# Kernel tuning notes

Measured on AMD Instinct MI355X. Metric: run time of the kernel, lower is better.

Reference implementation:

```python
import jax, jax.numpy as jnp
import numpy as np

B, S, DIM = 2, 2048, 512
NH, QK, VD = 8, 128, 128
NEG = -1e9


def setup_inputs() -> dict:
    key = jax.random.key(0)
    ks = jax.random.split(key, 10)
    scale = 0.02
    x = jax.random.normal(ks[0], (B, S, DIM), dtype=jnp.float32)
    pos_embedding = jax.random.normal(ks[1], (NH, S, S), dtype=jnp.float32) * scale
    # causal additive mask: 0 on/below diagonal, large negative above
    mask = jnp.where(jnp.tril(jnp.ones((S, S), dtype=bool)), 0.0, NEG).astype(jnp.float32)
    wq_w = jax.random.normal(ks[2], (DIM, NH * QK), dtype=jnp.float32) * scale
    wq_b = jax.random.normal(ks[3], (NH * QK,), dtype=jnp.float32) * scale
    wk_w = jax.random.normal(ks[4], (DIM, NH * QK), dtype=jnp.float32) * scale
    wk_b = jax.random.normal(ks[5], (NH * QK,), dtype=jnp.float32) * scale
    wv_w = jax.random.normal(ks[6], (DIM, NH * VD), dtype=jnp.float32) * scale
    wv_b = jax.random.normal(ks[7], (NH * VD,), dtype=jnp.float32) * scale
    wo_w = jax.random.normal(ks[8], (NH * VD, DIM), dtype=jnp.float32) * scale
    wo_b = jax.random.normal(ks[9], (DIM,), dtype=jnp.float32) * scale
    return {
        "x": x, "start_pos": 0, "mask": mask, "pos_embedding": pos_embedding,
        "wq_w": wq_w, "wq_b": wq_b, "wk_w": wk_w, "wk_b": wk_b,
        "wv_w": wv_w, "wv_b": wv_b, "wo_w": wo_w, "wo_b": wo_b,
    }


def reference(x, start_pos, mask, pos_embedding,
              wq_w, wq_b, wk_w, wk_b, wv_w, wv_b, wo_w, wo_b):
    b, s, _ = x.shape
    # per-head positional bias slice [NH, s, s]
    pe = pos_embedding[:, start_pos:start_pos + s, start_pos:start_pos + s]
    q = (x @ wq_w + wq_b).reshape(b, s, NH, QK)
    k = (x @ wk_w + wk_b).reshape(b, s, NH, QK)
    v = (x @ wv_w + wv_b).reshape(b, s, NH, VD)
    # unfused attention: full [b, h, s, S] score tensor
    score = jnp.einsum('bshk,bShk->bhsS', q, k) / np.float32(np.sqrt(QK))
    score = score + pe[None] + mask[None, None, :s, :s]
    score = jax.nn.softmax(score, axis=-1).astype(x.dtype)
    out = jnp.einsum('bhsS,bShv->bshv', score, v).reshape(b, s, NH * VD)
    return out @ wo_w + wo_b
```

## Files before the change

### kernel.cpp

```cpp
#include <hip/hip_runtime.h>
#include <hip/hip_bf16.h>
#include <stdint.h>

#define BB_ 2
#define SS_ 2048
#define DIM_ 512
#define NH_ 8
#define QK_ 128
#define VD_ 128

typedef __attribute__((ext_vector_type(8))) short bf16x8;
typedef __attribute__((ext_vector_type(4))) float f32x4;
typedef __attribute__((ext_vector_type(8))) unsigned short ushort8;
typedef __attribute__((ext_vector_type(4))) unsigned short ushort4v;

__device__ __forceinline__ unsigned short f2bf(float f) {
  union { float f; unsigned int u; } v; v.f = f;
  unsigned int r = v.u + 0x7FFFu + ((v.u >> 16) & 1u);
  return (unsigned short)(r >> 16);
}

__device__ __forceinline__ float bf2f(unsigned short u) {
  union { unsigned int u; float f; } v; v.u = ((unsigned int)u) << 16;
  return v.f;
}

__device__ __forceinline__ f32x4 mfma16(bf16x8 a, bf16x8 b, f32x4 c) {
  return __builtin_amdgcn_mfma_f32_16x16x32_bf16(a, b, c, 0, 0, 0);
}


__device__ void transpose_tile(const float* __restrict__ src, unsigned short* __restrict__ dst,
                               int R, int C, int c0, int r0, int tid, float (*t)[65]) {
  const int rr = tid >> 4, cc4 = (tid & 15) * 4;
#pragma unroll
  for (int p = 0; p < 4; p++) {
    float4 v = *reinterpret_cast<const float4*>(src + (size_t)(r0 + rr + p * 16) * C + c0 + cc4);
    t[rr + p * 16][cc4 + 0] = v.x; t[rr + p * 16][cc4 + 1] = v.y;
    t[rr + p * 16][cc4 + 2] = v.z; t[rr + p * 16][cc4 + 3] = v.w;
  }
  __syncthreads();
  const int cl = tid >> 2, rb = (tid & 3) * 16;
#pragma unroll
  for (int g = 0; g < 2; g++) {
    ushort8 o;
#pragma unroll
    for (int j = 0; j < 8; j++) o[j] = f2bf(t[rb + g * 8 + j][cl]);
    *reinterpret_cast<ushort8*>(dst + (size_t)(c0 + cl) * R + r0 + rb + g * 8) = o;
  }
}

__global__ void k_prep(const float* __restrict__ x, unsigned short* __restrict__ xb,
                       const float* __restrict__ wq, const float* __restrict__ wk,
                       const float* __restrict__ wv, unsigned short* __restrict__ wqkv_t,
                       const float* __restrict__ wo, unsigned short* __restrict__ wo_t,
                       const float* __restrict__ bq, const float* __restrict__ bk,
                       const float* __restrict__ bv, float* __restrict__ bias_out) {
  __shared__ float t[64][65];
  const int bid = blockIdx.x, tid = threadIdx.x;
  if (bid < 2048) {
    const int i = bid * 256 + tid;
    float4 v = reinterpret_cast<const float4*>(x)[i];
    ushort4v o;
    o[0] = f2bf(v.x); o[1] = f2bf(v.y); o[2] = f2bf(v.z); o[3] = f2bf(v.w);
    reinterpret_cast<ushort4v*>(xb)[i] = o;
  } else if (bid < 2432) {
    const int tt0 = bid - 2048;
    const int w = tt0 >> 7, tt = tt0 & 127;
    const float* src = (w == 0) ? wq : (w == 1) ? wk : wv;
    transpose_tile(src, wqkv_t + (size_t)w * 1024 * 512, 512, 1024,
                   (tt & 15) * 64, (tt >> 4) * 64, tid, t);
  } else if (bid < 2560) {
    const int tt = bid - 2432;
    transpose_tile(wo, wo_t, 1024, 512, (tt & 7) * 64, (tt >> 3) * 64, tid, t);
  } else {
    const int i = (bid - 2560) * 256 + tid;
    if (i < 1024) bias_out[i] = bq[i];
    else if (i < 2048) bias_out[i] = bk[i - 1024];
    else if (i < 3072) bias_out[i] = bv[i - 2048];
  }
}


template <int EPI>
__global__ __launch_bounds__(256) void k_gemm_bt(
    const unsigned short* __restrict__ A, const unsigned short* __restrict__ BT,
    const float* __restrict__ bias, int K,
    unsigned short* __restrict__ oq, unsigned short* __restrict__ ok,
    unsigned short* __restrict__ ovt, float* __restrict__ of) {
  __shared__ __align__(16) unsigned short Al[128][32];
  __shared__ __align__(16) unsigned short Bl[128][32];
  const int tid = threadIdx.x;
  const int lane = tid & 63, wave = tid >> 6;
  const int wm = wave >> 1, wn = wave & 1;
  const int lr = lane & 15, lg = lane >> 4;
  const int m0 = blockIdx.y * 128, n0 = blockIdx.x * 128;
  f32x4 acc[4][4] = {};
  const int srow = lane >> 2, scol = (lane & 3) * 8;

  for (int k0 = 0; k0 < K; k0 += 32) {
    __syncthreads();
    {
      const unsigned short* ga = A + (size_t)(m0 + wave * 16 + srow) * K + k0 + scol;
      __builtin_amdgcn_global_load_lds((const unsigned int*)ga,
                                       (unsigned int*)&Al[wave * 16][0], 16, 0, 0);
      __builtin_amdgcn_global_load_lds((const unsigned int*)(ga + (size_t)64 * K),
                                       (unsigned int*)&Al[wave * 16 + 64][0], 16, 0, 0);
      const unsigned short* gb = BT + (size_t)(n0 + wave * 16 + srow) * K + k0 + scol;
      __builtin_amdgcn_global_load_lds((const unsigned int*)gb,
                                       (unsigned int*)&Bl[wave * 16][0], 16, 0, 0);
      __builtin_amdgcn_global_load_lds((const unsigned int*)(gb + (size_t)64 * K),
                                       (unsigned int*)&Bl[wave * 16 + 64][0], 16, 0, 0);
    }
    __syncthreads();
    bf16x8 af[4], bfr[4];
#pragma unroll
    for (int i = 0; i < 4; i++)
      af[i] = *reinterpret_cast<const bf16x8*>(&Al[wm * 64 + i * 16 + lr][lg * 8]);
#pragma unroll
    for (int i = 0; i < 4; i++)
      bfr[i] = *reinterpret_cast<const bf16x8*>(&Bl[wn * 64 + i * 16 + lr][lg * 8]);
#pragma unroll
    for (int i = 0; i < 4; i++)
#pragma unroll
      for (int j = 0; j < 4; j++)
        acc[i][j] = mfma16(af[i], bfr[j], acc[i][j]);
  }

#pragma unroll
  for (int i = 0; i < 4; i++) {
#pragma unroll
    for (int j = 0; j < 4; j++) {
      const int n = n0 + wn * 64 + j * 16 + lr;
      const float bv = bias[n];
      const int mb = m0 + wm * 64 + i * 16 + lg * 4;
      if (EPI == 0) {
        const int region = n >> 10;
        const int h = (n & 1023) >> 7, d = n & 127;
        const int bb = mb >> 11, s0 = mb & 2047;
        const size_t hb = (size_t)(bb * NH_ + h) << 18;
        if (region == 2) {
          ushort4v pk;
#pragma unroll
          for (int r = 0; r < 4; r++) pk[r] = f2bf(acc[i][j][r] + bv);
          const int s32 = s0 >> 5, sg = (s0 >> 3) & 3, e0 = s0 & 7;
          const size_t off = hb + (size_t)(((s32 * 8 + (d >> 4)) * 4 + sg) * 128 + (d & 15) * 8 + e0);
          *reinterpret_cast<ushort4v*>(ovt + off) = pk;
        } else {
          unsigned short* dst = ((region == 0) ? oq : ok) + hb;
          const float qs = (region == 0) ? 0.08838834764831845f : 1.0f;
          const int rt_ = s0 >> 4, c_ = d >> 5, lg_ = (d >> 3) & 3, e_ = d & 7;
          const int lrb = s0 & 15;
#pragma unroll
          for (int r = 0; r < 4; r++)
            dst[(size_t)(((rt_ * 4 + c_) * 64 + lg_ * 16 + lrb + r) * 8 + e_)] =
                f2bf((acc[i][j][r] + bv) * qs);
        }
      } else {
#pragma unroll
        for (int r = 0; r < 4; r++) {
          const int m = mb + r;
          of[(size_t)m * DIM_ + n] = acc[i][j][r] + bv;
        }
      }
    }
  }
}


__global__ __launch_bounds__(256, 2) void k_attn(
    const unsigned short* __restrict__ q, const unsigned short* __restrict__ k,
    const unsigned short* __restrict__ vt, const float* __restrict__ pe,
    unsigned short* __restrict__ att) {
  __shared__ __align__(16) unsigned short P[4][2][16][72];
  __shared__ __align__(16) unsigned short Xo[4][32][136];
  __shared__ float Xml[4][32];

  const int h = blockIdx.x, p = blockIdx.y, b = blockIdx.z;
  const int lane = threadIdx.x & 63, wave = threadIdx.x >> 6;
  const int lr = lane & 15, lg = lane >> 4;

  const size_t hb = (size_t)(b * NH_ + h) << 18;
  const unsigned short* qfp = q + hb;
  const unsigned short* kfp = k + hb;
  const unsigned short* vfp = vt + hb;
  const float* peh = pe + (size_t)h * SS_ * SS_;

  for (int phase = 0; phase < 2; phase++) {
    const int rt = phase ? (63 - p) : p;
    const int myq0 = rt * 32 + lr;
    const float* pep = peh + (size_t)myq0 * SS_;

    bf16x8 qf[2][4];
#pragma unroll
    for (int t = 0; t < 2; t++)
#pragma unroll
      for (int c = 0; c < 4; c++)
        qf[t][c] = *reinterpret_cast<const bf16x8*>(
            qfp + ((size_t)((rt * 2 + t) * 4 + c) << 9) + (lane << 3));

    f32x4 o[2][8] = {};
    float l[2] = {0.f, 0.f};

    const int nkt = (rt >> 1) + 1;
    const int kt_lo = (nkt * wave) >> 2;
    const int kt_hi = (nkt * (wave + 1)) >> 2;

    for (int kt = kt_lo; kt < kt_hi; kt++) {
      const int kbase = kt * 64;

      f32x4 sc[2][4];
#pragma unroll
      for (int t = 0; t < 2; t++)
#pragma unroll
        for (int ck = 0; ck < 4; ck++)
          sc[t][ck] = *reinterpret_cast<const f32x4*>(
              pep + (size_t)(t * 16) * SS_ + kbase + ck * 16 + lg * 4);

      __builtin_amdgcn_s_setprio(1);
#pragma unroll
      for (int ck = 0; ck < 4; ck++) {
#pragma unroll
        for (int c = 0; c < 4; c++) {
          const bf16x8 kf = *reinterpret_cast<const bf16x8*>(
              kfp + ((size_t)((kt * 4 + ck) * 4 + c) << 9) + (lane << 3));
          sc[0][ck] = mfma16(kf, qf[0][c], sc[0][ck]);
          sc[1][ck] = mfma16(kf, qf[1][c], sc[1][ck]);
        }
      }
      __builtin_amdgcn_s_setprio(0);

      bf16x8 vf[8];
#pragma unroll
      for (int sub = 0; sub < 8; sub++)
        vf[sub] = *reinterpret_cast<const bf16x8*>(
            vfp + ((size_t)((kt * 2) * 8 + sub) << 9) + (lane << 3));

      const bool diag = (kt == nkt - 1);
#pragma unroll
      for (int t = 0; t < 2; t++) {
        const int mq = myq0 + t * 16;
        float rs0 = 0.f, rs1 = 0.f;
#pragma unroll
        for (int ck = 0; ck < 4; ck++) {
#pragma unroll
          for (int r = 0; r < 4; r++) {
            float v = sc[t][ck][r];
            if (diag && (kbase + ck * 16 + lg * 4 + r) > mq) v = -1e30f;
            const float pv = __expf(v);
            sc[t][ck][r] = pv;
            if (ck & 1) rs1 += pv; else rs0 += pv;
          }
        }
        l[t] += rs0 + rs1;
#pragma unroll
        for (int ck = 0; ck < 4; ck++) {
          ushort4v pk;
#pragma unroll
          for (int r = 0; r < 4; r++) pk[r] = f2bf(sc[t][ck][r]);
          *reinterpret_cast<ushort4v*>(&P[wave][t][lr][ck * 16 + lg * 4]) = pk;
        }
      }

      __builtin_amdgcn_s_setprio(1);
#pragma unroll
      for (int t = 0; t < 2; t++) {
        const bf16x8 pf = *reinterpret_cast<const bf16x8*>(&P[wave][t][lr][lg * 8]);
#pragma unroll
        for (int sub = 0; sub < 8; sub++)
          o[t][sub] = mfma16(vf[sub], pf, o[t][sub]);
      }
      __builtin_amdgcn_s_setprio(0);
#pragma unroll
      for (int sub = 0; sub < 8; sub++)
        vf[sub] = *reinterpret_cast<const bf16x8*>(
            vfp + ((size_t)((kt * 2 + 1) * 8 + sub) << 9) + (lane << 3));
      __builtin_amdgcn_s_setprio(1);
#pragma unroll
      for (int t = 0; t < 2; t++) {
        const bf16x8 pf = *reinterpret_cast<const bf16x8*>(&P[wave][t][lr][32 + lg * 8]);
#pragma unroll
        for (int sub = 0; sub < 8; sub++)
          o[t][sub] = mfma16(vf[sub], pf, o[t][sub]);
      }
      __builtin_amdgcn_s_setprio(0);
    }

#pragma unroll
    for (int t = 0; t < 2; t++) {
      l[t] += __shfl_xor(l[t], 16);
      l[t] += __shfl_xor(l[t], 32);
    }

#pragma unroll
    for (int t = 0; t < 2; t++) {
      const float inv = (l[t] > 0.f) ? 1.0f / l[t] : 0.f;
#pragma unroll
      for (int sub = 0; sub < 8; sub++) {
        ushort4v pk;
#pragma unroll
        for (int r = 0; r < 4; r++) pk[r] = f2bf(o[t][sub][r] * inv);
        *reinterpret_cast<ushort4v*>(&Xo[wave][t * 16 + lr][sub * 16 + lg * 4]) = pk;
      }
      if (lg == 0) Xml[wave][t * 16 + lr] = l[t];
    }
    __syncthreads();

    {
      const int mrow = wave * 8 + (lane >> 3);
      float c[4], csum = 0.f;
#pragma unroll
      for (int w = 0; w < 4; w++) { c[w] = Xml[w][mrow]; csum += c[w]; }
      const float invT = 1.0f / csum;
#pragma unroll
      for (int half = 0; half < 2; half++) {
        const int dc = (lane & 7) + half * 8;
        float acc[8] = {};
#pragma unroll
        for (int w = 0; w < 4; w++) {
          const ushort8 v = *reinterpret_cast<const ushort8*>(&Xo[w][mrow][dc * 8]);
#pragma unroll
          for (int e = 0; e < 8; e++) acc[e] += c[w] * bf2f(v[e]);
        }
        ushort8 outv;
#pragma unroll
        for (int e = 0; e < 8; e++) outv[e] = f2bf(acc[e] * invT);
        *reinterpret_cast<ushort8*>(
            att + (size_t)(b * SS_ + rt * 32 + mrow) * (NH_ * VD_) + h * VD_ + dc * 8) = outv;
      }
    }
    __syncthreads();
  }
}


extern "C" void kernel_launch(void* const* d_in, const int* in_sizes, int n_in,
                              void* d_out, int out_size, void* d_ws, size_t ws_size,
                              hipStream_t stream) {
  const float* x    = (const float*)d_in[0];
  const float* pe   = (const float*)d_in[3];
  const float* wq_w = (const float*)d_in[4];
  const float* wq_b = (const float*)d_in[5];
  const float* wk_w = (const float*)d_in[6];
  const float* wk_b = (const float*)d_in[7];
  const float* wv_w = (const float*)d_in[8];
  const float* wv_b = (const float*)d_in[9];
  const float* wo_w = (const float*)d_in[10];
  const float* wo_b = (const float*)d_in[11];
  float* out = (float*)d_out;

  char* ws = (char*)d_ws;
  unsigned short* x_bf   = (unsigned short*)(ws);
  unsigned short* wqkv_t = (unsigned short*)(ws + 4194304);
  unsigned short* wo_t   = (unsigned short*)(ws + 7340032);
  float*          qkv_b  = (float*)(ws + 8388608);
  unsigned short* qb     = (unsigned short*)(ws + 8400896);
  unsigned short* kb     = (unsigned short*)(ws + 16789504);
  unsigned short* vtb    = (unsigned short*)(ws + 25178112);
  unsigned short* attb   = (unsigned short*)(ws + 33566720);

  k_prep<<<2572, 256, 0, stream>>>(x, x_bf, wq_w, wk_w, wv_w, wqkv_t,
                                   wo_w, wo_t, wq_b, wk_b, wv_b, qkv_b);

  dim3 g1(24, 32);
  k_gemm_bt<0><<<g1, 256, 0, stream>>>(x_bf, wqkv_t, qkv_b, 512, qb, kb, vtb, nullptr);

  dim3 g2(NH_, 32, BB_);
  k_attn<<<g2, 256, 0, stream>>>(qb, kb, vtb, pe, attb);

  dim3 g3(4, 32);
  k_gemm_bt<1><<<g3, 256, 0, stream>>>(attb, wo_t, wo_b, 1024, nullptr, nullptr, nullptr, out);
}
```

Measured before the change: 103.1 us.

## Split attention key range across six waves with aliased shared buffers

The attention block grows from 4 to 6 waves, each handling a sixth of the causal key tiles, so more waves are available to hide memory latency. The P staging buffer and the per-wave output buffer now share one aliased shared-memory array, which requires an extra barrier before the output stage. The score computation is also split into two half-tiles, and V loads are issued in groups of four to lower register pressure. The costs are a larger six-way final reduction, two idle waves during the combine, and possible load imbalance when a query tile has few key tiles to divide among six waves.

New measurement: 122.3 us. +18.7%, slower.

```diff
diff --git a/kernel.cpp b/kernel.cpp
--- a/kernel.cpp
+++ b/kernel.cpp
@@ -168,13 +168,15 @@
 }
 
 
-__global__ __launch_bounds__(256, 2) void k_attn(
+#define PIDX(w, t, r, c)  ((((w) * 2 + (t)) * 16 + (r)) * 72 + (c))
+#define XIDX(w, r, c)     (((w) * 32 + (r)) * 136 + (c))
+
+__global__ __launch_bounds__(384, 2) void k_attn(
     const unsigned short* __restrict__ q, const unsigned short* __restrict__ k,
     const unsigned short* __restrict__ vt, const float* __restrict__ pe,
     unsigned short* __restrict__ att) {
-  __shared__ __align__(16) unsigned short P[4][2][16][72];
-  __shared__ __align__(16) unsigned short Xo[4][32][136];
-  __shared__ float Xml[4][32];
+  __shared__ __align__(16) unsigned short SH[26112];
+  __shared__ float Xml[6][32];
 
   const int h = blockIdx.x, p = blockIdx.y, b = blockIdx.z;
   const int lane = threadIdx.x & 63, wave = threadIdx.x >> 6;
@@ -203,87 +205,83 @@
     float l[2] = {0.f, 0.f};
 
     const int nkt = (rt >> 1) + 1;
-    const int kt_lo = (nkt * wave) >> 2;
-    const int kt_hi = (nkt * (wave + 1)) >> 2;
+    const int kt_lo = (nkt * wave) / 6;
+    const int kt_hi = (nkt * (wave + 1)) / 6;
 
     for (int kt = kt_lo; kt < kt_hi; kt++) {
       const int kbase = kt * 64;
-
-      f32x4 sc[2][4];
-#pragma unroll
-      for (int t = 0; t < 2; t++)
-#pragma unroll
-        for (int ck = 0; ck < 4; ck++)
-          sc[t][ck] = *reinterpret_cast<const f32x4*>(
-              pep + (size_t)(t * 16) * SS_ + kbase + ck * 16 + lg * 4);
-
-      __builtin_amdgcn_s_setprio(1);
-#pragma unroll
-      for (int ck = 0; ck < 4; ck++) {
-#pragma unroll
-        for (int c = 0; c < 4; c++) {
-          const bf16x8 kf = *reinterpret_cast<const bf16x8*>(
-              kfp + ((size_t)((kt * 4 + ck) * 4 + c) << 9) + (lane << 3));
-          sc[0][ck] = mfma16(kf, qf[0][c], sc[0][ck]);
-          sc[1][ck] = mfma16(kf, qf[1][c], sc[1][ck]);
-        }
-      }
-      __builtin_amdgcn_s_setprio(0);
-
-      bf16x8 vf[8];
-#pragma unroll
-      for (int sub = 0; sub < 8; sub++)
-        vf[sub] = *reinterpret_cast<const bf16x8*>(
-            vfp + ((size_t)((kt * 2) * 8 + sub) << 9) + (lane << 3));
-
       const bool diag = (kt == nkt - 1);
-#pragma unroll
-      for (int t = 0; t < 2; t++) {
-        const int mq = myq0 + t * 16;
-        float rs0 = 0.f, rs1 = 0.f;
-#pragma unroll
-        for (int ck = 0; ck < 4; ck++) {
-#pragma unroll
-          for (int r = 0; r < 4; r++) {
-            float v = sc[t][ck][r];
-            if (diag && (kbase + ck * 16 + lg * 4 + r) > mq) v = -1e30f;
-            const float pv = __expf(v);
-            sc[t][ck][r] = pv;
-            if (ck & 1) rs1 += pv; else rs0 += pv;
+
+#pragma unroll
+      for (int ckh = 0; ckh < 2; ckh++) {
+        f32x4 sch[2][2];
+#pragma unroll
+        for (int t = 0; t < 2; t++)
+#pragma unroll
+          for (int cc = 0; cc < 2; cc++)
+            sch[t][cc] = *reinterpret_cast<const f32x4*>(
+                pep + (size_t)(t * 16) * SS_ + kbase + (ckh * 2 + cc) * 16 + lg * 4);
+
+        __builtin_amdgcn_s_setprio(1);
+#pragma unroll
+        for (int cc = 0; cc < 2; cc++) {
+          const int ck = ckh * 2 + cc;
+#pragma unroll
+          for (int c = 0; c < 4; c++) {
+            const bf16x8 kf = *reinterpret_cast<const bf16x8*>(
+                kfp + ((size_t)((kt * 4 + ck) * 4 + c) << 9) + (lane << 3));
+            sch[0][cc] = mfma16(kf, qf[0][c], sch[0][cc]);
+            sch[1][cc] = mfma16(kf, qf[1][c], sch[1][cc]);
           }
         }
-        l[t] += rs0 + rs1;
-#pragma unroll
-        for (int ck = 0; ck < 4; ck++) {
-          ushort4v pk;
-#pragma unroll
-          for (int r = 0; r < 4; r++) pk[r] = f2bf(sc[t][ck][r]);
-          *reinterpret_cast<ushort4v*>(&P[wave][t][lr][ck * 16 + lg * 4]) = pk;
-        }
-      }
-
-      __builtin_amdgcn_s_setprio(1);
-#pragma unroll
-      for (int t = 0; t < 2; t++) {
-        const bf16x8 pf = *reinterpret_cast<const bf16x8*>(&P[wave][t][lr][lg * 8]);
-#pragma unroll
-        for (int sub = 0; sub < 8; sub++)
-          o[t][sub] = mfma16(vf[sub], pf, o[t][sub]);
-      }
-      __builtin_amdgcn_s_setprio(0);
-#pragma unroll
-      for (int sub = 0; sub < 8; sub++)
-        vf[sub] = *reinterpret_cast<const bf16x8*>(
-            vfp + ((size_t)((kt * 2 + 1) * 8 + sub) << 9) + (lane << 3));
-      __builtin_amdgcn_s_setprio(1);
-#pragma unroll
-      for (int t = 0; t < 2; t++) {
-        const bf16x8 pf = *reinterpret_cast<const bf16x8*>(&P[wave][t][lr][32 + lg * 8]);
-#pragma unroll
-        for (int sub = 0; sub < 8; sub++)
-          o[t][sub] = mfma16(vf[sub], pf, o[t][sub]);
-      }
-      __builtin_amdgcn_s_setprio(0);
+        __builtin_amdgcn_s_setprio(0);
+
+#pragma unroll
+        for (int t = 0; t < 2; t++) {
+          const int mq = myq0 + t * 16;
+          float rs = 0.f;
+#pragma unroll
+          for (int cc = 0; cc < 2; cc++) {
+            const int ck = ckh * 2 + cc;
+#pragma unroll
+            for (int r = 0; r < 4; r++) {
+              float v = sch[t][cc][r];
+              if (diag && (kbase + ck * 16 + lg * 4 + r) > mq) v = -1e30f;
+              const float pv = __expf(v);
+              sch[t][cc][r] = pv;
+              rs += pv;
+            }
+            ushort4v pk;
+#pragma unroll
+            for (int r = 0; r < 4; r++) pk[r] = f2bf(sch[t][cc][r]);
+            *reinterpret_cast<ushort4v*>(&SH[PIDX(wave, t, lr, ck * 16 + lg * 4)]) = pk;
+          }
+          l[t] += rs;
+        }
+      }
+
+#pragma unroll
+      for (int kk = 0; kk < 2; kk++) {
+        bf16x8 pf[2];
+#pragma unroll
+        for (int t = 0; t < 2; t++)
+          pf[t] = *reinterpret_cast<const bf16x8*>(&SH[PIDX(wave, t, lr, kk * 32 + lg * 8)]);
+#pragma unroll
+        for (int sg = 0; sg < 2; sg++) {
+          bf16x8 vf4[4];
+#pragma unroll
+          for (int s4 = 0; s4 < 4; s4++)
+            vf4[s4] = *reinterpret_cast<const bf16x8*>(
+                vfp + ((size_t)((kt * 2 + kk) * 8 + sg * 4 + s4) << 9) + (lane << 3));
+          __builtin_amdgcn_s_setprio(1);
+#pragma unroll
+          for (int t = 0; t < 2; t++)
+#pragma unroll
+            for (int s4 = 0; s4 < 4; s4++)
+              o[t][sg * 4 + s4] = mfma16(vf4[s4], pf[t], o[t][sg * 4 + s4]);
+          __builtin_amdgcn_s_setprio(0);
+        }
+      }
     }
 
 #pragma unroll
@@ -292,6 +290,8 @@
       l[t] += __shfl_xor(l[t], 32);
     }
 
+    __syncthreads();
+
 #pragma unroll
     for (int t = 0; t < 2; t++) {
       const float inv = (l[t] > 0.f) ? 1.0f / l[t] : 0.f;
@@ -300,25 +300,25 @@
         ushort4v pk;
 #pragma unroll
         for (int r = 0; r < 4; r++) pk[r] = f2bf(o[t][sub][r] * inv);
-        *reinterpret_cast<ushort4v*>(&Xo[wave][t * 16 + lr][sub * 16 + lg * 4]) = pk;
+        *reinterpret_cast<ushort4v*>(&SH[XIDX(wave, t * 16 + lr, sub * 16 + lg * 4)]) = pk;
       }
       if (lg == 0) Xml[wave][t * 16 + lr] = l[t];
     }
     __syncthreads();
 
-    {
+    if (wave < 4) {
       const int mrow = wave * 8 + (lane >> 3);
-      float c[4], csum = 0.f;
-#pragma unroll
-      for (int w = 0; w < 4; w++) { c[w] = Xml[w][mrow]; csum += c[w]; }
+      float c[6], csum = 0.f;
+#pragma unroll
+      for (int w = 0; w < 6; w++) { c[w] = Xml[w][mrow]; csum += c[w]; }
       const float invT = 1.0f / csum;
 #pragma unroll
       for (int half = 0; half < 2; half++) {
         const int dc = (lane & 7) + half * 8;
         float acc[8] = {};
 #pragma unroll
-        for (int w = 0; w < 4; w++) {
-          const ushort8 v = *reinterpret_cast<const ushort8*>(&Xo[w][mrow][dc * 8]);
+        for (int w = 0; w < 6; w++) {
+          const ushort8 v = *reinterpret_cast<const ushort8*>(&SH[XIDX(w, mrow, dc * 8)]);
 #pragma unroll
           for (int e = 0; e < 8; e++) acc[e] += c[w] * bf2f(v[e]);
         }
@@ -366,7 +366,7 @@
   k_gemm_bt<0><<<g1, 256, 0, stream>>>(x_bf, wqkv_t, qkv_b, 512, qb, kb, vtb, nullptr);
 
   dim3 g2(NH_, 32, BB_);
-  k_attn<<<g2, 256, 0, stream>>>(qb, kb, vtb, pe, attb);
+  k_attn<<<g2, 384, 0, stream>>>(qb, kb, vtb, pe, attb);
 
   dim3 g3(4, 32);
   k_gemm_bt<1><<<g3, 256, 0, stream>>>(attb, wo_t, wo_b, 1024, nullptr, nullptr, nullptr, out);
```
